# Kernel tuning notes

Measured on AMD Instinct MI355X. Metric: run time of the kernel, lower is better.

Reference implementation:

```python
import jax, jax.numpy as jnp
import numpy as np

EMBED_DIM = 1024
NUM_HEAD = 16
HEAD_DIM = EMBED_DIM // NUM_HEAD


def _linear_params(key, in_dim, out_dim):
    kw, kb = jax.random.split(key)
    bound = 1.0 / np.sqrt(in_dim)
    W = jax.random.uniform(kw, (out_dim, in_dim), minval=-bound, maxval=bound, dtype=jnp.float32)
    b = jax.random.uniform(kb, (out_dim,), minval=-bound, maxval=bound, dtype=jnp.float32)
    return W, b


def setup_inputs() -> dict:
    key = jax.random.key(0)
    ks = jax.random.split(key, 7)
    N, S, E = 2, 2048, EMBED_DIM
    k = jax.random.normal(ks[0], (N, S, E), dtype=jnp.float32)
    q = jax.random.normal(ks[1], (N, S, E), dtype=jnp.float32)
    v = jax.random.normal(ks[2], (N, S, E), dtype=jnp.float32)
    Wk, bk = _linear_params(ks[3], E, E)
    Wq, bq = _linear_params(ks[4], E, E)
    Wv, bv = _linear_params(ks[5], E, E)
    Wo, bo = _linear_params(ks[6], E, E)
    return {"key": k, "query": q, "value": v,
            "Wk": Wk, "bk": bk, "Wq": Wq, "bq": bq,
            "Wv": Wv, "bv": bv, "Wo": Wo, "bo": bo}


def reference(key, query, value, Wk, bk, Wq, bq, Wv, bv, Wo, bo):
    N, S_in, E = key.shape
    S_out = query.shape[1]
    H, D = NUM_HEAD, HEAD_DIM
    # projections (torch Linear: x @ W.T + b), split heads -> [N, H, S, D]
    k = (key @ Wk.T + bk).reshape(N, S_in, H, D).transpose(0, 2, 1, 3)
    q = (query @ Wq.T + bq).reshape(N, S_out, H, D).transpose(0, 2, 1, 3)
    v = (value @ Wv.T + bv).reshape(N, S_in, H, D).transpose(0, 2, 1, 3)
    # unfused attention: full [N,H,S_out,S_in] score matrix, scale, softmax
    weight = jnp.einsum("nhqd,nhkd->nhqk", q, k) / jnp.sqrt(jnp.float32(D))
    weight = jax.nn.softmax(weight, axis=-1)
    attn = jnp.einsum("nhqk,nhkd->nhqd", weight, v)  # [N,H,S_out,D]
    attn = attn.transpose(0, 2, 1, 3).reshape(N, S_out, E)
    return attn @ Wo.T + bo
```

## Files before the change

### kernel.cpp

```cpp
#include <hip/hip_runtime.h>

constexpr int E  = 1024;
constexpr int NH = 16;
constexpr int HD = 64;
constexpr int S  = 2048;
constexpr int NB = 2;
constexpr int M  = NB * S;

typedef unsigned short u16;
typedef _Float16 f16;
typedef __attribute__((ext_vector_type(8))) _Float16 h8v;
typedef __attribute__((ext_vector_type(2))) __fp16 hp2v;
typedef __attribute__((ext_vector_type(4))) float f4v;

__device__ __forceinline__ f4v mfmaH(h8v a, h8v b, f4v c) {
    return __builtin_amdgcn_mfma_f32_16x16x32_f16(a, b, c, 0, 0, 0);
}
__device__ __forceinline__ u16 f16bits(float x) {
    union { f16 h; u16 u; } t; t.h = (f16)x; return t.u;
}
__device__ __forceinline__ unsigned pkrtz(float a, float b) {
    union { hp2v h; unsigned u; } t;
    t.h = __builtin_amdgcn_cvt_pkrtz(a, b);
    return t.u;
}
__device__ __forceinline__ float fexp2(float x) {
    float r;
    asm("v_exp_f32 %0, %1" : "=v"(r) : "v"(x));
    return r;
}
typedef const __attribute__((address_space(1))) void gvoid;
typedef __attribute__((address_space(3))) void lvoid;
__device__ __forceinline__ void load_lds16(const u16* g, u16* l) {
    __builtin_amdgcn_global_load_lds((gvoid*)g, (lvoid*)l, 16, 0, 0);
}

__global__ __launch_bounds__(256)
void cvt_f16(const float* __restrict__ q, const float* __restrict__ k,
             const float* __restrict__ v,
             const float* __restrict__ wq, const float* __restrict__ wk,
             const float* __restrict__ wv, const float* __restrict__ wo,
             u16* __restrict__ out)
{
    const size_t ME = (size_t)M * E, EE = (size_t)E * E;
    const int z = blockIdx.y;
    const float* src = (z == 0) ? q : (z == 1) ? k : (z == 2) ? v
                     : (z == 3) ? wq : (z == 4) ? wk : (z == 5) ? wv : wo;
    const size_t len = (z < 3) ? ME : EE;
    u16* dst = out + ((z < 3) ? (size_t)z * ME : 3 * ME + (size_t)(z - 3) * EE);
    for (size_t i = ((size_t)blockIdx.x * 256 + threadIdx.x) * 8; i < len;
         i += (size_t)gridDim.x * 256 * 8) {
        float4 a = *reinterpret_cast<const float4*>(src + i);
        float4 b = *reinterpret_cast<const float4*>(src + i + 4);
        h8v o;
        o[0] = (f16)a.x; o[1] = (f16)a.y; o[2] = (f16)a.z; o[3] = (f16)a.w;
        o[4] = (f16)b.x; o[5] = (f16)b.y; o[6] = (f16)b.z; o[7] = (f16)b.w;
        *reinterpret_cast<h8v*>(dst + i) = o;
    }
}

__device__ __forceinline__ void gemm16_core(const u16* __restrict__ A,
                                            const u16* __restrict__ W,
                                            int bm, int bn, u16* lds, f4v acc[4][4])
{
    const int tid  = threadIdx.x;
    const int lane = tid & 63;
    const int wid  = tid >> 6;
    const int g = lane >> 4, c = lane & 15;
    const int wr = wid >> 1, wc = wid & 1;
    const int lrow = lane >> 3;
    const int lslot = lane & 7;
    const int sslot = lslot ^ lrow;

    for (int k0 = 0; k0 < E; k0 += 64) {
        #pragma unroll
        for (int i = 0; i < 4; ++i) {
            int rbase = wid * 32 + i * 8;
            load_lds16(A + (size_t)(bm + rbase + lrow) * E + k0 + (sslot << 3),
                       &lds[rbase * 64]);
            load_lds16(W + (size_t)(bn + rbase + lrow) * E + k0 + (sslot << 3),
                       &lds[8192 + rbase * 64]);
        }
        __syncthreads();

        h8v a[4][2];
        #pragma unroll
        for (int mf = 0; mf < 4; ++mf) {
            int row = wr * 64 + mf * 16 + c;
            #pragma unroll
            for (int ks = 0; ks < 2; ++ks)
                a[mf][ks] = *reinterpret_cast<h8v*>(
                    &lds[row * 64 + ((((ks << 2) | g) ^ (c & 7)) << 3)]);
        }
        #pragma unroll
        for (int nf = 0; nf < 4; ++nf) {
            int row = wc * 64 + nf * 16 + c;
            #pragma unroll
            for (int ks = 0; ks < 2; ++ks) {
                h8v b = *reinterpret_cast<h8v*>(
                    &lds[8192 + row * 64 + ((((ks << 2) | g) ^ (c & 7)) << 3)]);
                #pragma unroll
                for (int mf = 0; mf < 4; ++mf)
                    acc[mf][nf] = mfmaH(a[mf][ks], b, acc[mf][nf]);
            }
        }
        __syncthreads();
    }
}

__global__ __launch_bounds__(256, 3)
void qkv_gemm(const u16* __restrict__ qf, const u16* __restrict__ kf,
              const u16* __restrict__ vf,
              const u16* __restrict__ wqf, const u16* __restrict__ wkf,
              const u16* __restrict__ wvf,
              const float* __restrict__ bq, const float* __restrict__ bk,
              const float* __restrict__ bv,
              u16* __restrict__ Qattn, u16* __restrict__ KV, float scaleQ)
{
    __shared__ __align__(16) u16 lds[16384];
    const int z = blockIdx.z;
    const u16* A = (z == 0) ? qf : (z == 1) ? kf : vf;
    const u16* W = (z == 0) ? wqf : (z == 1) ? wkf : wvf;
    const float* bias = (z == 0) ? bq : (z == 1) ? bk : bv;
    const float scl = (z == 0) ? scaleQ : 1.0f;
    const int bm = blockIdx.x * 128, bn = blockIdx.y * 128;

    f4v acc[4][4];
    #pragma unroll
    for (int a = 0; a < 4; ++a)
        #pragma unroll
        for (int b = 0; b < 4; ++b) acc[a][b] = (f4v){0.f, 0.f, 0.f, 0.f};

    gemm16_core(A, W, bm, bn, lds, acc);

    const int lane = threadIdx.x & 63;
    const int g = lane >> 4, c = lane & 15;
    const int wid = threadIdx.x >> 6;
    const int wr = wid >> 1, wc = wid & 1;
    float bcol[4];
    #pragma unroll
    for (int nf = 0; nf < 4; ++nf) bcol[nf] = bias[bn + wc * 64 + nf * 16 + c];

    #pragma unroll
    for (int mf = 0; mf < 4; ++mf)
        #pragma unroll
        for (int r = 0; r < 4; ++r) {
            int m  = bm + wr * 64 + mf * 16 + g * 4 + r;
            int nb = m >> 11, sp = m & (S - 1);
            #pragma unroll
            for (int nf = 0; nf < 4; ++nf) {
                int ncol = bn + wc * 64 + nf * 16 + c;
                int h = ncol >> 6, d = ncol & 63;
                int bh_ = nb * NH + h;
                u16 hb = f16bits((acc[mf][nf][r] + bcol[nf]) * scl);
                if (z == 0) {
                    Qattn[((size_t)bh_ * S + sp) * HD + d] = hb;
                } else if (z == 1) {
                    int t = sp >> 6, kk = (sp >> 4) & 3, cc = sp & 15;
                    int ds = d >> 5, gg = (d >> 3) & 3, j = d & 7;
                    KV[((size_t)bh_ * 32 + t) * 8192 +
                       ((size_t)((kk * 2 + ds) * 64 + gg * 16 + cc)) * 8 + j] = hb;
                } else {
                    int t = sp >> 6, rem = sp & 63;
                    int s2 = rem >> 5, bb = (rem >> 4) & 1, gg = (rem >> 2) & 3, a2 = rem & 3;
                    int j = 4 * bb + a2;
                    int df = d >> 4, cc = d & 15;
                    KV[((size_t)bh_ * 32 + t) * 8192 + 4096 +
                       ((size_t)((df * 2 + s2) * 64 + gg * 16 + cc)) * 8 + j] = hb;
                }
            }
        }
}

__global__ __launch_bounds__(256, 3)
void out_gemm(const u16* __restrict__ A, const u16* __restrict__ W,
              const float* __restrict__ bias, float* __restrict__ C)
{
    __shared__ __align__(16) u16 lds[16384];
    const int bm = blockIdx.x * 128, bn = blockIdx.y * 128;
    f4v acc[4][4];
    #pragma unroll
    for (int a = 0; a < 4; ++a)
        #pragma unroll
        for (int b = 0; b < 4; ++b) acc[a][b] = (f4v){0.f, 0.f, 0.f, 0.f};

    gemm16_core(A, W, bm, bn, lds, acc);

    const int lane = threadIdx.x & 63;
    const int g = lane >> 4, c = lane & 15;
    const int wid = threadIdx.x >> 6;
    const int wr = wid >> 1, wc = wid & 1;
    float bcol[4];
    #pragma unroll
    for (int nf = 0; nf < 4; ++nf) bcol[nf] = bias[bn + wc * 64 + nf * 16 + c];

    #pragma unroll
    for (int mf = 0; mf < 4; ++mf)
        #pragma unroll
        for (int r = 0; r < 4; ++r) {
            int m = bm + wr * 64 + mf * 16 + g * 4 + r;
            float* crow = &C[(size_t)m * E + bn + wc * 64];
            #pragma unroll
            for (int nf = 0; nf < 4; ++nf)
                crow[nf * 16 + c] = acc[mf][nf][r] + bcol[nf];
        }
}

__global__ __launch_bounds__(128, 2)
void attn_mfma(const u16* __restrict__ Qf, const u16* __restrict__ KV,
               u16* __restrict__ Out)
{
    __shared__ __align__(16) u16 lds[16384];
    const int tid  = threadIdx.x;
    const int lane = tid & 63;
    const int wid  = tid >> 6;
    const int g = lane >> 4, c = lane & 15;
    const int dlin = blockIdx.x;
    const int idx  = dlin >> 3;
    const int bh = (dlin & 7) * 4 + (idx >> 5);
    const int qc = idx & 31;
    const int n = bh >> 4, h = bh & 15;
    const int q0 = qc * 64 + wid * 32;
    const u16* kvb = KV + (size_t)bh * 32 * 8192;
    const f4v zero4 = {0.f, 0.f, 0.f, 0.f};

    h8v Qb[2][2];
    #pragma unroll
    for (int qf = 0; qf < 2; ++qf)
        #pragma unroll
        for (int ds = 0; ds < 2; ++ds)
            Qb[qf][ds] = *reinterpret_cast<const h8v*>(
                &Qf[((size_t)bh * S + q0 + qf * 16 + c) * HD + ds * 32 + g * 8]);

    h8v ones;
    #pragma unroll
    for (int i = 0; i < 8; ++i) ones[i] = (f16)1.0f;

    f4v oacc[2][4];
    #pragma unroll
    for (int qf = 0; qf < 2; ++qf)
        #pragma unroll
        for (int df = 0; df < 4; ++df) oacc[qf][df] = zero4;
    f4v lacc[2] = {zero4, zero4};

    #pragma unroll
    for (int tt = 0; tt < 2; ++tt) {
        const u16* src = kvb + tt * 8192 + wid * 4096 + lane * 8;
        u16* dst = &lds[tt * 8192 + wid * 4096];
        #pragma unroll
        for (int i = 0; i < 8; ++i) load_lds16(src + i * 512, dst + i * 512);
    }

    int cur = 0;
    #define ATTN_TILE_BODY(BT)                                                  \
    {                                                                           \
        const u16* Bt = (BT);                                                   \
                                    \
        h8v vh[4][2];                                                           \
        _Pragma("unroll")                                                       \
        for (int df = 0; df < 4; ++df)                                          \
            _Pragma("unroll")                                                   \
            for (int s2 = 0; s2 < 2; ++s2)                                      \
                vh[df][s2] = *reinterpret_cast<const h8v*>(                     \
                    &Bt[4096 + ((size_t)((df * 2 + s2) * 64 + lane)) * 8]);     \
        f4v sc[2][4];                                                           \
        _Pragma("unroll")                                                       \
        for (int qf = 0; qf < 2; ++qf)                                          \
            _Pragma("unroll")                                                   \
            for (int kf = 0; kf < 4; ++kf) sc[qf][kf] = zero4;                  \
        __builtin_amdgcn_s_setprio(1);                                          \
        _Pragma("unroll")                                                       \
        for (int kf = 0; kf < 4; ++kf) {                                        \
            _Pragma("unroll")                                                   \
            for (int ds = 0; ds < 2; ++ds) {                                    \
                h8v kh = *reinterpret_cast<const h8v*>(                         \
                    &Bt[((size_t)((kf * 2 + ds) * 64 + lane)) * 8]);            \
                _Pragma("unroll")                                               \
                for (int qf = 0; qf < 2; ++qf)                                  \
                    sc[qf][kf] = mfmaH(kh, Qb[qf][ds], sc[qf][kf]);             \
            }                                                                   \
        }                                                                       \
        __builtin_amdgcn_s_setprio(0);                                          \
        h8v pah[2][2];                                                          \
        _Pragma("unroll")                                                       \
        for (int qf = 0; qf < 2; ++qf)                                          \
            _Pragma("unroll")                                                   \
            for (int s2 = 0; s2 < 2; ++s2) {                                    \
                union { h8v v; unsigned u[4]; } th;                             \
                _Pragma("unroll")                                               \
                for (int kfh = 0; kfh < 2; ++kfh) {                             \
                    int kf = 2 * s2 + kfh;                                      \
                    float p0 = fexp2(sc[qf][kf][0]);                            \
                    float p1 = fexp2(sc[qf][kf][1]);                            \
                    float p2 = fexp2(sc[qf][kf][2]);                            \
                    float p3 = fexp2(sc[qf][kf][3]);                            \
                    th.u[2 * kfh + 0] = pkrtz(p0, p1);                          \
                    th.u[2 * kfh + 1] = pkrtz(p2, p3);                          \
                }                                                               \
                pah[qf][s2] = th.v;                                             \
            }                                                                   \
        __builtin_amdgcn_s_setprio(1);                                          \
        _Pragma("unroll")                                                       \
        for (int qf = 0; qf < 2; ++qf) {                                        \
            lacc[qf] = mfmaH(pah[qf][0], ones, lacc[qf]);                       \
            lacc[qf] = mfmaH(pah[qf][1], ones, lacc[qf]);                       \
        }                                                                       \
        _Pragma("unroll")                                                       \
        for (int df = 0; df < 4; ++df)                                          \
            _Pragma("unroll")                                                   \
            for (int s2 = 0; s2 < 2; ++s2)                                      \
                _Pragma("unroll")                                               \
                for (int qf = 0; qf < 2; ++qf)                                  \
                    oacc[qf][df] = mfmaH(pah[qf][s2], vh[df][s2], oacc[qf][df]);\
        __builtin_amdgcn_s_setprio(0);                                          \
    }

    for (int t = 0; t < 31; ++t) {
        asm volatile("s_waitcnt vmcnt(8)" ::: "memory");
        __builtin_amdgcn_s_barrier();
        ATTN_TILE_BODY(&lds[cur * 8192]);
        __builtin_amdgcn_s_barrier();
        if (t < 30) {
            const u16* src = kvb + (size_t)(t + 2) * 8192 + wid * 4096 + lane * 8;
            u16* dst = &lds[cur * 8192 + wid * 4096];
            #pragma unroll
            for (int i = 0; i < 8; ++i) load_lds16(src + i * 512, dst + i * 512);
        }
        cur ^= 1;
    }
    asm volatile("s_waitcnt vmcnt(0)" ::: "memory");
    __builtin_amdgcn_s_barrier();
    ATTN_TILE_BODY(&lds[cur * 8192]);
    #undef ATTN_TILE_BODY

    #pragma unroll
    for (int qf = 0; qf < 2; ++qf)
        #pragma unroll
        for (int r = 0; r < 4; ++r) {
            float linv = 1.0f / lacc[qf][r];
            int q = q0 + qf * 16 + g * 4 + r;
            size_t ob = ((size_t)n * S + q) * E + h * HD;
            #pragma unroll
            for (int df = 0; df < 4; ++df)
                Out[ob + df * 16 + c] = f16bits(oacc[qf][df][r] * linv);
        }
}

extern "C" void kernel_launch(void* const* d_in, const int* in_sizes, int n_in,
                              void* d_out, int out_size, void* d_ws, size_t ws_size,
                              hipStream_t stream)
{
    const float* key   = (const float*)d_in[0];
    const float* query = (const float*)d_in[1];
    const float* value = (const float*)d_in[2];
    const float* Wk    = (const float*)d_in[3];
    const float* bk    = (const float*)d_in[4];
    const float* Wq    = (const float*)d_in[5];
    const float* bq    = (const float*)d_in[6];
    const float* Wv    = (const float*)d_in[7];
    const float* bv    = (const float*)d_in[8];
    const float* Wo    = (const float*)d_in[9];
    const float* bo    = (const float*)d_in[10];

    const size_t ME = (size_t)M * E, EE = (size_t)E * E;
    u16* ws16  = (u16*)d_ws;
    u16* qf16  = ws16;
    u16* kf16  = ws16 + ME;
    u16* vf16  = ws16 + 2 * ME;
    u16* wqf   = ws16 + 3 * ME;
    u16* wkf   = wqf + EE;
    u16* wvf   = wkf + EE;
    u16* wof   = wvf + EE;
    u16* Qattn = wof + EE;
    u16* KV    = Qattn + ME;
    u16* AoutH = ws16;

    const float SCALE_Q = 0.125f * 1.44269504088896340736f;

    cvt_f16<<<dim3(2048, 7), 256, 0, stream>>>(query, key, value, Wq, Wk, Wv, Wo, ws16);
    qkv_gemm<<<dim3(M / 128, E / 128, 3), 256, 0, stream>>>(
        qf16, kf16, vf16, wqf, wkf, wvf, bq, bk, bv, Qattn, KV, SCALE_Q);
    attn_mfma<<<dim3((S / 64) * NB * NH), 128, 0, stream>>>(Qattn, KV, AoutH);
    out_gemm<<<dim3(M / 128, E / 128), 256, 0, stream>>>(AoutH, wof, bo, (float*)d_out);
}
```

Before: 116.3 us.

## Software-pipeline attention loop: overlap QK of next tile with softmax/PV of previous

Restructures the attention inner loop into a two-stage software pipeline. Each phase computes the QK scores for the current tile while doing exp, row-sum and PV for the previous tile's scores, which are held in registers. V fragments are copied from LDS to registers early so the buffer can be refilled sooner. The aim is to interleave exp/VALU work with MFMA and hide dependency latency, at the cost of more live registers (two score sets and two V sets), which may reduce occupancy.

```diff
diff --git a/kernel.cpp b/kernel.cpp
--- a/kernel.cpp
+++ b/kernel.cpp
@@ -243,43 +243,71 @@
         for (int df = 0; df < 4; ++df) oacc[qf][df] = zero4;
     f4v lacc[2] = {zero4, zero4};
 
-    #pragma unroll
-    for (int tt = 0; tt < 2; ++tt) {
-        const u16* src = kvb + tt * 8192 + wid * 4096 + lane * 8;
-        u16* dst = &lds[tt * 8192 + wid * 4096];
-        #pragma unroll
-        for (int i = 0; i < 8; ++i) load_lds16(src + i * 512, dst + i * 512);
-    }
-
-    int cur = 0;
-    #define ATTN_TILE_BODY(BT)                                                  \
+    f4v scA[2][4], scB[2][4];
+    h8v vrA[4][2], vrB[4][2];
+
+    #define STAGE(T, BUFOFF)                                                    \
     {                                                                           \
-        const u16* Bt = (BT);                                                   \
-                                    \
-        h8v vh[4][2];                                                           \
-        _Pragma("unroll")                                                       \
-        for (int df = 0; df < 4; ++df)                                          \
-            _Pragma("unroll")                                                   \
-            for (int s2 = 0; s2 < 2; ++s2)                                      \
-                vh[df][s2] = *reinterpret_cast<const h8v*>(                     \
-                    &Bt[4096 + ((size_t)((df * 2 + s2) * 64 + lane)) * 8]);     \
-        f4v sc[2][4];                                                           \
+        const u16* src = kvb + (size_t)(T) * 8192 + wid * 4096 + lane * 8;      \
+        u16* dst = &lds[(BUFOFF) + wid * 4096];                                 \
+        _Pragma("unroll")                                                       \
+        for (int i = 0; i < 8; ++i) load_lds16(src + i * 512, dst + i * 512);   \
+    }
+
+    STAGE(0, 0);
+    STAGE(1, 8192);
+
+    asm volatile("s_waitcnt vmcnt(8)" ::: "memory");
+    __builtin_amdgcn_s_barrier();
+    {
+        const u16* Bt = &lds[0];
+        #pragma unroll
+        for (int qf = 0; qf < 2; ++qf)
+            #pragma unroll
+            for (int kf = 0; kf < 4; ++kf) scA[qf][kf] = zero4;
+        __builtin_amdgcn_s_setprio(1);
+        #pragma unroll
+        for (int kf = 0; kf < 4; ++kf)
+            #pragma unroll
+            for (int ds = 0; ds < 2; ++ds) {
+                h8v kh = *reinterpret_cast<const h8v*>(
+                    &Bt[((size_t)((kf * 2 + ds) * 64 + lane)) * 8]);
+                #pragma unroll
+                for (int qf = 0; qf < 2; ++qf)
+                    scA[qf][kf] = mfmaH(kh, Qb[qf][ds], scA[qf][kf]);
+            }
+        __builtin_amdgcn_s_setprio(0);
+        #pragma unroll
+        for (int df = 0; df < 4; ++df)
+            #pragma unroll
+            for (int s2 = 0; s2 < 2; ++s2)
+                vrA[df][s2] = *reinterpret_cast<const h8v*>(
+                    &Bt[4096 + ((size_t)((df * 2 + s2) * 64 + lane)) * 8]);
+    }
+    asm volatile("s_waitcnt lgkmcnt(0)" ::: "memory");
+    __builtin_amdgcn_s_barrier();
+    STAGE(2, 0);
+
+    #define PHASE(T, BUFOFF, SCP, SCC, VRP, VRC, WAITN)                         \
+    asm volatile("s_waitcnt vmcnt(" WAITN ")" ::: "memory");                    \
+    __builtin_amdgcn_s_barrier();                                               \
+    {                                                                           \
+        const u16* Bt = &lds[BUFOFF];                                           \
         _Pragma("unroll")                                                       \
         for (int qf = 0; qf < 2; ++qf)                                          \
             _Pragma("unroll")                                                   \
-            for (int kf = 0; kf < 4; ++kf) sc[qf][kf] = zero4;                  \
+            for (int kf = 0; kf < 4; ++kf) SCC[qf][kf] = zero4;                 \
         __builtin_amdgcn_s_setprio(1);                                          \
         _Pragma("unroll")                                                       \
-        for (int kf = 0; kf < 4; ++kf) {                                        \
+        for (int kf = 0; kf < 4; ++kf)                                          \
             _Pragma("unroll")                                                   \
             for (int ds = 0; ds < 2; ++ds) {                                    \
                 h8v kh = *reinterpret_cast<const h8v*>(                         \
                     &Bt[((size_t)((kf * 2 + ds) * 64 + lane)) * 8]);            \
                 _Pragma("unroll")                                               \
                 for (int qf = 0; qf < 2; ++qf)                                  \
-                    sc[qf][kf] = mfmaH(kh, Qb[qf][ds], sc[qf][kf]);             \
+                    SCC[qf][kf] = mfmaH(kh, Qb[qf][ds], SCC[qf][kf]);           \
             }                                                                   \
-        }                                                                       \
         __builtin_amdgcn_s_setprio(0);                                          \
         h8v pah[2][2];                                                          \
         _Pragma("unroll")                                                       \
@@ -290,10 +318,10 @@
                 _Pragma("unroll")                                               \
                 for (int kfh = 0; kfh < 2; ++kfh) {                             \
                     int kf = 2 * s2 + kfh;                                      \
-                    float p0 = fexp2(sc[qf][kf][0]);                            \
-                    float p1 = fexp2(sc[qf][kf][1]);                            \
-                    float p2 = fexp2(sc[qf][kf][2]);                            \
-                    float p3 = fexp2(sc[qf][kf][3]);                            \
+                    float p0 = fexp2(SCP[qf][kf][0]);                           \
+                    float p1 = fexp2(SCP[qf][kf][1]);                           \
+                    float p2 = fexp2(SCP[qf][kf][2]);                           \
+                    float p3 = fexp2(SCP[qf][kf][3]);                           \
                     th.u[2 * kfh + 0] = pkrtz(p0, p1);                          \
                     th.u[2 * kfh + 1] = pkrtz(p2, p3);                          \
                 }                                                               \
@@ -311,27 +339,60 @@
             for (int s2 = 0; s2 < 2; ++s2)                                      \
                 _Pragma("unroll")                                               \
                 for (int qf = 0; qf < 2; ++qf)                                  \
-                    oacc[qf][df] = mfmaH(pah[qf][s2], vh[df][s2], oacc[qf][df]);\
+                    oacc[qf][df] = mfmaH(pah[qf][s2], VRP[df][s2],              \
+                                         oacc[qf][df]);                         \
         __builtin_amdgcn_s_setprio(0);                                          \
-    }
-
-    for (int t = 0; t < 31; ++t) {
-        asm volatile("s_waitcnt vmcnt(8)" ::: "memory");
-        __builtin_amdgcn_s_barrier();
-        ATTN_TILE_BODY(&lds[cur * 8192]);
-        __builtin_amdgcn_s_barrier();
-        if (t < 30) {
-            const u16* src = kvb + (size_t)(t + 2) * 8192 + wid * 4096 + lane * 8;
-            u16* dst = &lds[cur * 8192 + wid * 4096];
-            #pragma unroll
-            for (int i = 0; i < 8; ++i) load_lds16(src + i * 512, dst + i * 512);
-        }
-        cur ^= 1;
-    }
-    asm volatile("s_waitcnt vmcnt(0)" ::: "memory");
-    __builtin_amdgcn_s_barrier();
-    ATTN_TILE_BODY(&lds[cur * 8192]);
-    #undef ATTN_TILE_BODY
+        _Pragma("unroll")                                                       \
+        for (int df = 0; df < 4; ++df)                                          \
+            _Pragma("unroll")                                                   \
+            for (int s2 = 0; s2 < 2; ++s2)                                      \
+                VRC[df][s2] = *reinterpret_cast<const h8v*>(                    \
+                    &Bt[4096 + ((size_t)((df * 2 + s2) * 64 + lane)) * 8]);     \
+    }                                                                           \
+    asm volatile("s_waitcnt lgkmcnt(0)" ::: "memory");                          \
+    __builtin_amdgcn_s_barrier();                                               \
+    if ((T) + 2 < 32) STAGE((T) + 2, BUFOFF)
+
+    for (int t = 1; t < 31; t += 2) {
+        PHASE(t,     8192, scA, scB, vrA, vrB, "8");
+        PHASE(t + 1, 0,    scB, scA, vrB, vrA, "8");
+    }
+    PHASE(31, 8192, scA, scB, vrA, vrB, "0");
+    #undef PHASE
+    #undef STAGE
+
+    {
+        h8v pah[2][2];
+        #pragma unroll
+        for (int qf = 0; qf < 2; ++qf)
+            #pragma unroll
+            for (int s2 = 0; s2 < 2; ++s2) {
+                union { h8v v; unsigned u[4]; } th;
+                #pragma unroll
+                for (int kfh = 0; kfh < 2; ++kfh) {
+                    int kf = 2 * s2 + kfh;
+                    float p0 = fexp2(scB[qf][kf][0]);
+                    float p1 = fexp2(scB[qf][kf][1]);
+                    float p2 = fexp2(scB[qf][kf][2]);
+                    float p3 = fexp2(scB[qf][kf][3]);
+                    th.u[2 * kfh + 0] = pkrtz(p0, p1);
+                    th.u[2 * kfh + 1] = pkrtz(p2, p3);
+                }
+                pah[qf][s2] = th.v;
+            }
+        #pragma unroll
+        for (int qf = 0; qf < 2; ++qf) {
+            lacc[qf] = mfmaH(pah[qf][0], ones, lacc[qf]);
+            lacc[qf] = mfmaH(pah[qf][1], ones, lacc[qf]);
+        }
+        #pragma unroll
+        for (int df = 0; df < 4; ++df)
+            #pragma unroll
+            for (int s2 = 0; s2 < 2; ++s2)
+                #pragma unroll
+                for (int qf = 0; qf < 2; ++qf)
+                    oacc[qf][df] = mfmaH(pah[qf][s2], vrB[df][s2], oacc[qf][df]);
+    }
 
     #pragma unroll
     for (int qf = 0; qf < 2; ++qf)
```

Result: no change. 115.4 us (-0.7%).

## Process two KV tiles per phase, staging only K in LDS and prefetching V to registers

Applied to the files above, without the earlier changes.

The attention loop now handles two 64-key tiles per phase (16 phases instead of 32), halving barrier count. Only K is staged through LDS by asynchronous global-to-LDS copies, while V for the next phase is loaded straight from global memory into registers and overlaps with the current phase's compute. The vmcnt wait counts are retuned to match this mixed load stream. This raises register pressure (twice as many scores and V fragments held) and relies on the hand-set waitcnt values being correct.

```diff
diff --git a/kernel.cpp b/kernel.cpp
--- a/kernel.cpp
+++ b/kernel.cpp
@@ -243,95 +243,108 @@
         for (int df = 0; df < 4; ++df) oacc[qf][df] = zero4;
     f4v lacc[2] = {zero4, zero4};
 
-    #pragma unroll
-    for (int tt = 0; tt < 2; ++tt) {
-        const u16* src = kvb + tt * 8192 + wid * 4096 + lane * 8;
-        u16* dst = &lds[tt * 8192 + wid * 4096];
-        #pragma unroll
-        for (int i = 0; i < 8; ++i) load_lds16(src + i * 512, dst + i * 512);
-    }
-
-    int cur = 0;
-    #define ATTN_TILE_BODY(BT)                                                  \
+    h8v vh[4][4];
+
+    #define STAGE_K2(P, BUFOFF)                                                 \
     {                                                                           \
-        const u16* Bt = (BT);                                                   \
-                                    \
-        h8v vh[4][2];                                                           \
+        const u16* src = kvb + (size_t)(2 * (P) + wid) * 8192 + lane * 8;       \
+        u16* dst = &lds[(BUFOFF) + wid * 4096];                                 \
+        _Pragma("unroll")                                                       \
+        for (int i = 0; i < 8; ++i) load_lds16(src + i * 512, dst + i * 512);   \
+    }
+    #define VLOAD2(P)                                                           \
+    {                                                                           \
         _Pragma("unroll")                                                       \
         for (int df = 0; df < 4; ++df)                                          \
             _Pragma("unroll")                                                   \
-            for (int s2 = 0; s2 < 2; ++s2)                                      \
+            for (int s2 = 0; s2 < 4; ++s2)                                      \
                 vh[df][s2] = *reinterpret_cast<const h8v*>(                     \
-                    &Bt[4096 + ((size_t)((df * 2 + s2) * 64 + lane)) * 8]);     \
-        f4v sc[2][4];                                                           \
+                    &kvb[(size_t)(2 * (P) + (s2 >> 1)) * 8192 + 4096 +          \
+                         ((size_t)((df * 2 + (s2 & 1)) * 64 + lane)) * 8]);     \
+    }
+
+    #define PHASE2(P, BUFOFF, WAITN)                                            \
+    asm volatile("s_waitcnt vmcnt(" WAITN ")" ::: "memory");                    \
+    __builtin_amdgcn_s_barrier();                                               \
+    {                                                                           \
+        const u16* Bt = &lds[BUFOFF];                                           \
+        f4v sc[2][8];                                                           \
         _Pragma("unroll")                                                       \
         for (int qf = 0; qf < 2; ++qf)                                          \
             _Pragma("unroll")                                                   \
-            for (int kf = 0; kf < 4; ++kf) sc[qf][kf] = zero4;                  \
+            for (int kf = 0; kf < 8; ++kf) sc[qf][kf] = zero4;                  \
         __builtin_amdgcn_s_setprio(1);                                          \
         _Pragma("unroll")                                                       \
-        for (int kf = 0; kf < 4; ++kf) {                                        \
+        for (int kf = 0; kf < 8; ++kf) {                                        \
+            int st = kf >> 2, lkf = kf & 3;                                     \
             _Pragma("unroll")                                                   \
             for (int ds = 0; ds < 2; ++ds) {                                    \
                 h8v kh = *reinterpret_cast<const h8v*>(                         \
-                    &Bt[((size_t)((kf * 2 + ds) * 64 + lane)) * 8]);            \
+                    &Bt[st * 4096 +                                             \
+                        ((size_t)((lkf * 2 + ds) * 64 + lane)) * 8]);           \
                 _Pragma("unroll")                                               \
                 for (int qf = 0; qf < 2; ++qf)                                  \
                     sc[qf][kf] = mfmaH(kh, Qb[qf][ds], sc[qf][kf]);             \
             }                                                                   \
         }                                                                       \
         __builtin_amdgcn_s_setprio(0);                                          \
-        h8v pah[2][2];                                                          \
-        _Pragma("unroll")                                                       \
-        for (int qf = 0; qf < 2; ++qf)                                          \
-            _Pragma("unroll")                                                   \
-            for (int s2 = 0; s2 < 2; ++s2) {                                    \
-                union { h8v v; unsigned u[4]; } th;                             \
+        _Pragma("unroll")                                                       \
+        for (int half = 0; half < 2; ++half) {                                  \
+            h8v pah[2][2];                                                      \
+            _Pragma("unroll")                                                   \
+            for (int qf = 0; qf < 2; ++qf)                                      \
                 _Pragma("unroll")                                               \
-                for (int kfh = 0; kfh < 2; ++kfh) {                             \
-                    int kf = 2 * s2 + kfh;                                      \
-                    float p0 = fexp2(sc[qf][kf][0]);                            \
-                    float p1 = fexp2(sc[qf][kf][1]);                            \
-                    float p2 = fexp2(sc[qf][kf][2]);                            \
-                    float p3 = fexp2(sc[qf][kf][3]);                            \
-                    th.u[2 * kfh + 0] = pkrtz(p0, p1);                          \
-                    th.u[2 * kfh + 1] = pkrtz(p2, p3);                          \
+                for (int s2l = 0; s2l < 2; ++s2l) {                             \
+                    int s2 = half * 2 + s2l;                                    \
+                    union { h8v v; unsigned u[4]; } th;                         \
+                    _Pragma("unroll")                                           \
+                    for (int kfh = 0; kfh < 2; ++kfh) {                         \
+                        int kf = 2 * s2 + kfh;                                  \
+                        float p0 = fexp2(sc[qf][kf][0]);                        \
+                        float p1 = fexp2(sc[qf][kf][1]);                        \
+                        float p2 = fexp2(sc[qf][kf][2]);                        \
+                        float p3 = fexp2(sc[qf][kf][3]);                        \
+                        th.u[2 * kfh + 0] = pkrtz(p0, p1);                      \
+                        th.u[2 * kfh + 1] = pkrtz(p2, p3);                      \
+                    }                                                           \
+                    pah[qf][s2l] = th.v;                                        \
                 }                                                               \
-                pah[qf][s2] = th.v;                                             \
+            __builtin_amdgcn_s_setprio(1);                                      \
+            _Pragma("unroll")                                                   \
+            for (int qf = 0; qf < 2; ++qf) {                                    \
+                lacc[qf] = mfmaH(pah[qf][0], ones, lacc[qf]);                   \
+                lacc[qf] = mfmaH(pah[qf][1], ones, lacc[qf]);                   \
             }                                                                   \
-        __builtin_amdgcn_s_setprio(1);                                          \
-        _Pragma("unroll")                                                       \
-        for (int qf = 0; qf < 2; ++qf) {                                        \
-            lacc[qf] = mfmaH(pah[qf][0], ones, lacc[qf]);                       \
-            lacc[qf] = mfmaH(pah[qf][1], ones, lacc[qf]);                       \
+            _Pragma("unroll")                                                   \
+            for (int df = 0; df < 4; ++df)                                      \
+                _Pragma("unroll")                                               \
+                for (int s2l = 0; s2l < 2; ++s2l)                               \
+                    _Pragma("unroll")                                           \
+                    for (int qf = 0; qf < 2; ++qf)                              \
+                        oacc[qf][df] = mfmaH(pah[qf][s2l],                      \
+                                             vh[df][half * 2 + s2l],            \
+                                             oacc[qf][df]);                     \
+            __builtin_amdgcn_s_setprio(0);                                      \
         }                                                                       \
-        _Pragma("unroll")                                                       \
-        for (int df = 0; df < 4; ++df)                                          \
-            _Pragma("unroll")                                                   \
-            for (int s2 = 0; s2 < 2; ++s2)                                      \
-                _Pragma("unroll")                                               \
-                for (int qf = 0; qf < 2; ++qf)                                  \
-                    oacc[qf][df] = mfmaH(pah[qf][s2], vh[df][s2], oacc[qf][df]);\
-        __builtin_amdgcn_s_setprio(0);                                          \
-    }
-
-    for (int t = 0; t < 31; ++t) {
-        asm volatile("s_waitcnt vmcnt(8)" ::: "memory");
-        __builtin_amdgcn_s_barrier();
-        ATTN_TILE_BODY(&lds[cur * 8192]);
-        __builtin_amdgcn_s_barrier();
-        if (t < 30) {
-            const u16* src = kvb + (size_t)(t + 2) * 8192 + wid * 4096 + lane * 8;
-            u16* dst = &lds[cur * 8192 + wid * 4096];
-            #pragma unroll
-            for (int i = 0; i < 8; ++i) load_lds16(src + i * 512, dst + i * 512);
-        }
-        cur ^= 1;
-    }
-    asm volatile("s_waitcnt vmcnt(0)" ::: "memory");
-    __builtin_amdgcn_s_barrier();
-    ATTN_TILE_BODY(&lds[cur * 8192]);
-    #undef ATTN_TILE_BODY
+        if ((P) + 1 < 16) VLOAD2((P) + 1);                                      \
+    }                                                                           \
+    __builtin_amdgcn_s_barrier();                                               \
+    if ((P) + 2 < 16) STAGE_K2((P) + 2, BUFOFF)
+
+    VLOAD2(0);
+    STAGE_K2(0, 0);
+    STAGE_K2(1, 8192);
+
+    PHASE2(0, 0, "8");
+    for (int p = 1; p < 15; p += 2) {
+        PHASE2(p,     8192, "24");
+        PHASE2(p + 1, 0,    "24");
+    }
+    PHASE2(15, 8192, "16");
+
+    #undef PHASE2
+    #undef STAGE_K2
+    #undef VLOAD2
 
     #pragma unroll
     for (int qf = 0; qf < 2; ++qf)
```

Result: no change. 116.9 us (+0.5%).
